# Performance work log

Measured on AMD Instinct MI355X. Metric: run time of the kernel, lower is better.

Reference implementation:

```python
import jax, jax.numpy as jnp
import numpy as np

V0, V1, V2 = 2000, 1500, 500   # diag / proc / med vocab sizes
D = 256                        # emb_dim
T = 16                         # visits per patient (query and memory)
P = 512                        # memory-bank patients
LD, LP, LM = 24, 16, 24        # codes per visit per type
PAD = V0 + V1 + V2             # padding row index (zeroed)
THRESH = 0.8
EPS = 1e-6


def setup_inputs() -> dict:
    key = jax.random.key(0)
    ks = jax.random.split(key, 16)
    inp = {
        "q_diag": jax.random.randint(ks[0], (T, LD), 0, V0),
        "q_proc": jax.random.randint(ks[1], (T, LP), 0, V1),
        "q_med": jax.random.randint(ks[2], (T, LM), 0, V2),
        "mem_diag": jax.random.randint(ks[3], (P, T, LD), 0, V0),
        "mem_proc": jax.random.randint(ks[4], (P, T, LP), 0, V1),
        "mem_med": jax.random.randint(ks[5], (P, T, LM), 0, V2),
        "emb": (jax.random.normal(ks[6], (PAD + 1, D)) * 0.05).at[PAD].set(0.0),
        "Wih": jax.random.normal(ks[7], (3 * D, D)) * 0.05,
        "Whh": jax.random.normal(ks[8], (3 * D, D)) * 0.05,
        "bih": jax.random.normal(ks[9], (3 * D,)) * 0.05,
        "bhh": jax.random.normal(ks[10], (3 * D,)) * 0.05,
        "W2": jax.random.normal(ks[11], (D, D)) * 0.05,
        "b2": jax.random.normal(ks[12], (D,)) * 0.05,
        "Wo": jax.random.normal(ks[13], (V2, D)) * 0.05,
        "bo": jax.random.normal(ks[14], (V2,)) * 0.05,
        "k": 16,
    }
    return inp


def _run_gru(x, Wih, Whh, bih, bhh):
    # x: [B, T, D]; torch nn.GRU gate order: r, z, n
    xT = jnp.swapaxes(x, 0, 1)                      # [T, B, D]
    gx = xT @ Wih.T + bih                           # [T, B, 3D]
    h0 = jnp.zeros(x.shape[:1] + x.shape[2:], x.dtype)  # [B, D]

    def step(h, gx_t):
        gh = h @ Whh.T + bhh
        xr, xz, xn = jnp.split(gx_t, 3, axis=-1)
        hr, hz, hn = jnp.split(gh, 3, axis=-1)
        r = jax.nn.sigmoid(xr + hr)
        z = jax.nn.sigmoid(xz + hz)
        n = jnp.tanh(xn + r * hn)
        h_new = (1.0 - z) * n + z * h
        return h_new, h_new

    _, hs = jax.lax.scan(step, h0, gx)
    return jnp.swapaxes(hs, 0, 1)                   # [B, T, D]


def _encode_visits(diag, proc, med, emb, Wih, Whh, bih, bhh, W2, b2):
    # diag/proc/med: [B, T, L*] int. Returns encoders for visits 1..T-1: [B, T-1, D].
    e_d = emb[diag].sum(axis=2)                     # [B, T, D]
    e_p = emb[proc + V0].sum(axis=2)
    e_m = emb[med + V0 + V1].sum(axis=2)
    e_nomed = e_d + e_p                             # current visit excludes meds
    e_full = e_nomed + e_m                          # history visits include meds
    h = _run_gru(e_full, Wih, Whh, bih, bhh)        # [B, T, D]
    # attn_g = softmax over size-1 axis == 1 exactly, so encoder_1 drops out.
    terms = jnp.tanh(h @ W2.T + b2) * e_full        # [B, T, D]
    c = jnp.cumsum(terms, axis=1)                   # prefix context sums
    return c[:, :-1] + e_nomed[:, 1:]               # enc_i = c_{i-1..} + current_i


def reference(q_diag, q_proc, q_med, mem_diag, mem_proc, mem_med,
              emb, Wih, Whh, bih, bhh, W2, b2, Wo, bo, k):
    gru = (Wih, Whh, bih, bhh)
    # Memory bank: every prefix encoder of every memory patient -> [P*(T-1), D]
    M = _encode_visits(mem_diag, mem_proc, mem_med, emb, *gru, W2, b2)
    M = M.reshape(-1, D)
    # Query patient prefix encoders -> [T-1, D]
    Q = _encode_visits(q_diag[None], q_proc[None], q_med[None], emb, *gru, W2, b2)[0]
    # Cosine similarity (torch CosineSimilarity, eps=1e-6)
    qn = jnp.maximum(jnp.linalg.norm(Q, axis=-1, keepdims=True), EPS)
    mn = jnp.maximum(jnp.linalg.norm(M, axis=-1, keepdims=True), EPS)
    sims = (Q / qn) @ (M / mn).T                    # [T-1, Nmem]
    vals, idx = jax.lax.top_k(sims, k)              # [T-1, k]
    w = jnp.where(vals > THRESH, vals, 0.0)         # threshold mask
    gathered = M[idx]                               # [T-1, k, D]
    out = Q + jnp.einsum("qk,qkd->qd", w, gathered) # weighted gather-sum
    return jax.nn.sigmoid(out @ Wo.T + bo)          # [T-1, V2]
```

## Files before the change

### kernel.cpp

```cpp
#include <hip/hip_runtime.h>
#include <math.h>

constexpr int V0_ = 2000, V1_ = 1500, V2_ = 500;
constexpr int D_ = 256, T_ = 16, P_ = 512;
constexpr int LD_ = 24, LP_ = 16, LM_ = 24;
constexpr int NPAT = P_ + 1;
constexpr int NV   = NPAT * T_;
constexpr int NM   = P_ * (T_ - 1);
constexpr int NQ   = T_ - 1;
constexpr int NROWS = NPAT * NQ;
constexpr float THRESH_ = 0.8f;
constexpr float EPS_ = 1e-6f;

__device__ __forceinline__ float sigmoidf_(float x) { return 1.0f / (1.0f + expf(-x)); }

__global__ void embed_kernel(const int* __restrict__ qd, const int* __restrict__ qp,
                             const int* __restrict__ qm, const int* __restrict__ md,
                             const int* __restrict__ mp, const int* __restrict__ mm,
                             const float* __restrict__ emb,
                             float* __restrict__ e_nomed, float* __restrict__ e_full) {
  int b = blockIdx.x;
  int p = b / T_, t = b % T_;
  int tid = threadIdx.x;
  __shared__ int codes[64];
  if (tid < 64) {
    int c;
    if (tid < LD_) {
      c = (p < P_) ? md[(p * T_ + t) * LD_ + tid] : qd[t * LD_ + tid];
    } else if (tid < LD_ + LP_) {
      int i = tid - LD_;
      c = ((p < P_) ? mp[(p * T_ + t) * LP_ + i] : qp[t * LP_ + i]) + V0_;
    } else {
      int i = tid - LD_ - LP_;
      c = ((p < P_) ? mm[(p * T_ + t) * LM_ + i] : qm[t * LM_ + i]) + V0_ + V1_;
    }
    codes[tid] = c;
  }
  __syncthreads();
  float s0 = 0.f, s1 = 0.f;
  #pragma unroll 8
  for (int i = 0; i < LD_ + LP_; ++i) s0 += emb[codes[i] * D_ + tid];
  #pragma unroll 8
  for (int i = LD_ + LP_; i < 64; ++i) s1 += emb[codes[i] * D_ + tid];
  e_nomed[(size_t)b * D_ + tid] = s0;
  e_full[(size_t)b * D_ + tid]  = s0 + s1;
}

#define BM 128
#define BN 64
#define BK 32
__global__ void gemm_nt_bias(const float* __restrict__ A, const float* __restrict__ B,
                             const float* __restrict__ bias, float* __restrict__ C,
                             int M, int N, int nct) {
  const int K = 256;
  __shared__ float As[BK][BM + 5];
  __shared__ float Bs[BK][BN + 5];
  int nb = gridDim.x;
  int b = blockIdx.x;
  int q = nb >> 3, r = nb & 7;
  int xcd = b & 7, i0 = b >> 3;
  int nbb = (xcd < r) ? (xcd * (q + 1) + i0) : (r * (q + 1) + (xcd - r) * q + i0);
  int rt = nbb / nct, ct = nbb - rt * nct;
  int r0 = rt * BM;
  int c0 = ct * BN;
  int tid = threadIdx.x;
  int tx = tid & 15, ty = tid >> 4;
  float acc[8][4];
  #pragma unroll
  for (int i = 0; i < 8; ++i)
    #pragma unroll
    for (int j = 0; j < 4; ++j) acc[i][j] = 0.f;

  for (int k0 = 0; k0 < K; k0 += BK) {
    #pragma unroll
    for (int i = 0; i < 4; ++i) {
      int flat = i * 256 + tid;
      int rr = flat >> 3;
      int kq = flat & 7;
      float4 v = make_float4(0.f, 0.f, 0.f, 0.f);
      if (r0 + rr < M) v = *(const float4*)(A + (size_t)(r0 + rr) * K + k0 + kq * 4);
      As[kq * 4 + 0][rr] = v.x; As[kq * 4 + 1][rr] = v.y;
      As[kq * 4 + 2][rr] = v.z; As[kq * 4 + 3][rr] = v.w;
    }
    #pragma unroll
    for (int i = 0; i < 2; ++i) {
      int flat = i * 256 + tid;
      int rr = flat >> 3;
      int kq = flat & 7;
      float4 v = *(const float4*)(B + (size_t)(c0 + rr) * K + k0 + kq * 4);
      Bs[kq * 4 + 0][rr] = v.x; Bs[kq * 4 + 1][rr] = v.y;
      Bs[kq * 4 + 2][rr] = v.z; Bs[kq * 4 + 3][rr] = v.w;
    }
    __syncthreads();
    #pragma unroll
    for (int kk = 0; kk < BK; ++kk) {
      float4 a0 = *(const float4*)&As[kk][ty * 8];
      float4 a1 = *(const float4*)&As[kk][ty * 8 + 4];
      float4 bv = *(const float4*)&Bs[kk][tx * 4];
      float av[8] = {a0.x, a0.y, a0.z, a0.w, a1.x, a1.y, a1.z, a1.w};
      float bw[4] = {bv.x, bv.y, bv.z, bv.w};
      #pragma unroll
      for (int i = 0; i < 8; ++i)
        #pragma unroll
        for (int j = 0; j < 4; ++j) acc[i][j] = fmaf(av[i], bw[j], acc[i][j]);
    }
    __syncthreads();
  }
  float bv0 = bias[c0 + tx * 4 + 0], bv1 = bias[c0 + tx * 4 + 1];
  float bv2 = bias[c0 + tx * 4 + 2], bv3 = bias[c0 + tx * 4 + 3];
  #pragma unroll
  for (int i = 0; i < 8; ++i) {
    int rr = r0 + ty * 8 + i;
    if (rr < M) {
      float4 o = make_float4(acc[i][0] + bv0, acc[i][1] + bv1,
                             acc[i][2] + bv2, acc[i][3] + bv3);
      *(float4*)(C + (size_t)rr * N + c0 + tx * 4) = o;
    }
  }
}

__global__ void transpose_whh(const float* __restrict__ Whh, float* __restrict__ WT) {
  int idx = blockIdx.x * 256 + threadIdx.x;
  int row = idx >> 8;
  int e = idx & 255;
  WT[e * 768 + row] = Whh[idx];
}

__global__ __launch_bounds__(512) void gru_all(const float* __restrict__ gx,
                                               const float* __restrict__ WT,
                                               const float* __restrict__ bhh,
                                               float* __restrict__ hs_all) {
  int tid = threadIdx.x;
  int d = tid & 255;
  int hf = tid >> 8;
  int p0 = blockIdx.x * 3;
  __shared__ float hL[3][D_];
  __shared__ float part[9][D_];
  if (hf == 0) { hL[0][d] = 0.f; hL[1][d] = 0.f; hL[2][d] = 0.f; }
  float brd = bhh[d], bzd = bhh[D_ + d], bnd = bhh[2 * D_ + d];
  __syncthreads();

  for (int t = 0; t < T_; ++t) {
    float ar[3] = {0.f, 0.f, 0.f}, az[3] = {0.f, 0.f, 0.f}, an[3] = {0.f, 0.f, 0.f};
    const float* wt = WT + d;
    int e0 = hf << 7;
    #pragma unroll 4
    for (int e = e0; e < e0 + 128; ++e) {
      const float* we = wt + (size_t)e * 768;
      float w0 = we[0];
      float w1 = we[256];
      float w2 = we[512];
      float h0 = hL[0][e], h1 = hL[1][e], h2 = hL[2][e];
      ar[0] = fmaf(h0, w0, ar[0]); az[0] = fmaf(h0, w1, az[0]); an[0] = fmaf(h0, w2, an[0]);
      ar[1] = fmaf(h1, w0, ar[1]); az[1] = fmaf(h1, w1, az[1]); an[1] = fmaf(h1, w2, an[1]);
      ar[2] = fmaf(h2, w0, ar[2]); az[2] = fmaf(h2, w1, az[2]); an[2] = fmaf(h2, w2, an[2]);
    }
    if (hf == 1) {
      #pragma unroll
      for (int i = 0; i < 3; ++i) {
        part[i][d] = ar[i]; part[3 + i][d] = az[i]; part[6 + i][d] = an[i];
      }
    }
    __syncthreads();
    if (hf == 0) {
      #pragma unroll
      for (int i = 0; i < 3; ++i) {
        int p = p0 + i;
        const float* gxp = gx + (size_t)(p * T_ + t) * 768;
        float r = sigmoidf_(gxp[d] + brd + ar[i] + part[i][d]);
        float z = sigmoidf_(gxp[D_ + d] + bzd + az[i] + part[3 + i][d]);
        float n = tanhf(gxp[2 * D_ + d] + r * (an[i] + part[6 + i][d] + bnd));
        float hn = (1.f - z) * n + z * hL[i][d];
        hL[i][d] = hn;
        hs_all[(size_t)(p * T_ + t) * D_ + d] = hn;
      }
    }
    __syncthreads();
  }
}

__global__ void enc_kernel(const float* __restrict__ tmp, const float* __restrict__ e_full,
                           const float* __restrict__ e_nomed, float* __restrict__ enc) {
  int p = blockIdx.x, d = threadIdx.x;
  float acc = 0.f;
  for (int t = 0; t < NQ; ++t) {
    size_t vi = (size_t)(p * T_ + t) * D_ + d;
    acc += tanhf(tmp[vi]) * e_full[vi];
    enc[(size_t)(p * NQ + t) * D_ + d] = acc + e_nomed[(size_t)(p * T_ + t + 1) * D_ + d];
  }
}

__global__ void norm_kernel(const float* __restrict__ enc, float* __restrict__ norms) {
  int row = blockIdx.x * 4 + (threadIdx.x >> 6);
  int lane = threadIdx.x & 63;
  if (row >= NROWS) return;
  const float* rp = enc + (size_t)row * D_;
  float s = 0.f;
  #pragma unroll
  for (int i = 0; i < 4; ++i) { float v = rp[lane + i * 64]; s += v * v; }
  #pragma unroll
  for (int off = 32; off > 0; off >>= 1) s += __shfl_down(s, off, 64);
  if (lane == 0) norms[row] = fmaxf(sqrtf(s), EPS_);
}

__global__ void sims_kernel(const float* __restrict__ enc, const float* __restrict__ norms,
                            float* __restrict__ sims) {
  int q = blockIdx.y;
  int m = blockIdx.x * 256 + threadIdx.x;
  __shared__ float qs[D_];
  qs[threadIdx.x] = enc[(size_t)(NM + q) * D_ + threadIdx.x];
  __syncthreads();
  const float* mrow = enc + (size_t)m * D_;
  float dot = 0.f;
  #pragma unroll 8
  for (int e = 0; e < D_; e += 4) {
    float4 a = *(const float4*)(qs + e);
    float4 b = *(const float4*)(mrow + e);
    dot += a.x * b.x + a.y * b.y + a.z * b.z + a.w * b.w;
  }
  sims[(size_t)q * NM + m] = dot / (norms[NM + q] * norms[m]);
}

#define CAP 4096
__global__ void topk_gather(const float* __restrict__ sims, const float* __restrict__ enc,
                            const int* __restrict__ kptr, float* __restrict__ outq) {
  int q = blockIdx.x, tid = threadIdx.x;
  __shared__ int cnt;
  __shared__ float cv[CAP];
  __shared__ int ci[CAP];
  __shared__ float selv[64];
  __shared__ int seli[64];
  __shared__ float rv[256];
  __shared__ int ri[256];
  if (tid == 0) cnt = 0;
  __syncthreads();
  const float* sq = sims + (size_t)q * NM;
  for (int j = tid; j < NM; j += 256) {
    float v = sq[j];
    if (v > THRESH_) {
      int slot = atomicAdd(&cnt, 1);
      if (slot < CAP) { cv[slot] = v; ci[slot] = j; }
    }
  }
  __syncthreads();
  int k = kptr[0];
  if (k > 64) k = 64;
  if (k < 0) k = 0;
  int n = cnt; if (n > CAP) n = CAP;
  int nsel;
  if (n <= k) {
    nsel = n;
    if (tid < n) { selv[tid] = cv[tid]; seli[tid] = ci[tid]; }
  } else {
    nsel = k;
    for (int it = 0; it < k; ++it) {
      float best = -3e38f; int bslot = -1;
      for (int j = tid; j < n; j += 256) {
        float v = cv[j];
        if (v > best) { best = v; bslot = j; }
        else if (v == best && bslot >= 0 && ci[j] < ci[bslot]) { bslot = j; }
      }
      rv[tid] = best; ri[tid] = bslot;
      __syncthreads();
      for (int off = 128; off > 0; off >>= 1) {
        if (tid < off) {
          float v2 = rv[tid + off]; int s2 = ri[tid + off];
          if (s2 >= 0 && (ri[tid] < 0 || v2 > rv[tid] ||
                          (v2 == rv[tid] && ci[s2] < ci[ri[tid]]))) {
            rv[tid] = v2; ri[tid] = s2;
          }
        }
        __syncthreads();
      }
      if (tid == 0) {
        int s = ri[0];
        selv[it] = rv[0]; seli[it] = ci[s];
        cv[s] = -3e38f;
      }
      __syncthreads();
    }
  }
  __syncthreads();
  float o = enc[(size_t)(NM + q) * D_ + tid];
  for (int j = 0; j < nsel; ++j)
    o += selv[j] * enc[(size_t)seli[j] * D_ + tid];
  outq[(size_t)q * D_ + tid] = o;
}

__global__ void out_kernel(const float* __restrict__ outq, const float* __restrict__ Wo,
                           const float* __restrict__ bo, float* __restrict__ out) {
  int q = blockIdx.y;
  int v = blockIdx.x * 256 + threadIdx.x;
  __shared__ float qs[D_];
  qs[threadIdx.x] = outq[(size_t)q * D_ + threadIdx.x];
  __syncthreads();
  if (v >= V2_) return;
  const float* wr = Wo + (size_t)v * D_;
  float dot = bo[v];
  #pragma unroll 8
  for (int e = 0; e < D_; e += 4) {
    float4 a = *(const float4*)(qs + e);
    float4 b = *(const float4*)(wr + e);
    dot += a.x * b.x + a.y * b.y + a.z * b.z + a.w * b.w;
  }
  out[(size_t)q * V2_ + v] = 1.f / (1.f + expf(-dot));
}

extern "C" void kernel_launch(void* const* d_in, const int* in_sizes, int n_in,
                              void* d_out, int out_size, void* d_ws, size_t ws_size,
                              hipStream_t stream) {
  const int* qd = (const int*)d_in[0];
  const int* qp = (const int*)d_in[1];
  const int* qm = (const int*)d_in[2];
  const int* md = (const int*)d_in[3];
  const int* mp = (const int*)d_in[4];
  const int* mm = (const int*)d_in[5];
  const float* emb = (const float*)d_in[6];
  const float* Wih = (const float*)d_in[7];
  const float* Whh = (const float*)d_in[8];
  const float* bih = (const float*)d_in[9];
  const float* bhh = (const float*)d_in[10];
  const float* W2  = (const float*)d_in[11];
  const float* b2  = (const float*)d_in[12];
  const float* Wo  = (const float*)d_in[13];
  const float* bo  = (const float*)d_in[14];
  const int* kptr  = (const int*)d_in[15];
  float* out = (float*)d_out;
  (void)in_sizes; (void)n_in; (void)out_size; (void)ws_size;

  char* ws = (char*)d_ws;
  size_t off = 0;
  auto alloc = [&](size_t nfloats) {
    float* pp = (float*)(ws + off);
    off += ((nfloats * sizeof(float) + 255) & ~(size_t)255);
    return pp;
  };
  float* e_full  = alloc((size_t)NV * D_);
  float* e_nomed = alloc((size_t)NV * D_);
  float* gx      = alloc((size_t)NV * 768);
  float* hs_all  = alloc((size_t)NV * D_);
  float* tmp     = alloc((size_t)NV * D_);
  float* enc     = alloc((size_t)NROWS * D_);
  float* norms   = alloc(NROWS);
  float* sims    = alloc((size_t)NQ * NM);
  float* outq    = alloc((size_t)NQ * D_);
  float* WT      = alloc((size_t)256 * 768);

  embed_kernel<<<NV, 256, 0, stream>>>(qd, qp, qm, md, mp, mm, emb, e_nomed, e_full);

  transpose_whh<<<768, 256, 0, stream>>>(Whh, WT);

  {
    int nrt = (NV + BM - 1) / BM, nct = 768 / BN;
    gemm_nt_bias<<<nrt * nct, 256, 0, stream>>>(e_full, Wih, bih, gx, NV, 768, nct);
  }

  gru_all<<<NPAT / 3, 512, 0, stream>>>(gx, WT, bhh, hs_all);

  {
    int nrt = (NV + BM - 1) / BM, nct = 256 / BN;
    gemm_nt_bias<<<nrt * nct, 256, 0, stream>>>(hs_all, W2, b2, tmp, NV, 256, nct);
  }

  enc_kernel<<<NPAT, 256, 0, stream>>>(tmp, e_full, e_nomed, enc);
  norm_kernel<<<(NROWS + 3) / 4, 256, 0, stream>>>(enc, norms);
  sims_kernel<<<dim3(NM / 256, NQ), 256, 0, stream>>>(enc, norms, sims);
  topk_gather<<<NQ, 256, 0, stream>>>(sims, enc, kptr, outq);
  out_kernel<<<dim3((V2_ + 255) / 256, NQ), 256, 0, stream>>>(outq, Wo, bo, out);
}
```

Before: 408.5 us.

## Vectorize GRU recurrent weights as float4, split K four ways, fuse norm into encoder

The transposed recurrent weight matrix is re-laid out into float4 groups so each GRU thread loads four k-values per gate at once, and the hidden-state reads from shared memory become float4. The recurrent matvec now splits K across four 256-thread quarters in 1024-thread blocks instead of two, with three partial-sum slabs reduced in shared memory. The row-norm computation moves into the encoder kernel through a wave shuffle plus block reduction, which removes one launch and a re-read of the encodings. In exchange the GRU uses more shared memory and larger blocks, and the encoder loop adds two barriers per step.

New measurement: 387.9 us. 5.0% less time.

```diff
diff --git a/kernel.cpp b/kernel.cpp
--- a/kernel.cpp
+++ b/kernel.cpp
@@ -119,57 +119,68 @@
   }
 }
 
-__global__ void transpose_whh(const float* __restrict__ Whh, float* __restrict__ WT) {
-  int idx = blockIdx.x * 256 + threadIdx.x;
-  int row = idx >> 8;
-  int e = idx & 255;
-  WT[e * 768 + row] = Whh[idx];
-}
-
-__global__ __launch_bounds__(512) void gru_all(const float* __restrict__ gx,
-                                               const float* __restrict__ WT,
-                                               const float* __restrict__ bhh,
-                                               float* __restrict__ hs_all) {
+__global__ void transpose_whh(const float* __restrict__ Whh, float* __restrict__ WT4) {
+  int b = blockIdx.x;
+  int e4 = b / 3, g = b - e4 * 3;
+  int d = threadIdx.x;
+  float4 v = *(const float4*)(Whh + ((size_t)(g * 256 + d)) * 256 + e4 * 4);
+  *((float4*)WT4 + (size_t)b * 256 + d) = v;
+}
+
+__global__ __launch_bounds__(1024) void gru_all(const float* __restrict__ gx,
+                                                const float* __restrict__ WT4,
+                                                const float* __restrict__ bhh,
+                                                float* __restrict__ hs_all) {
   int tid = threadIdx.x;
   int d = tid & 255;
-  int hf = tid >> 8;
+  int qt = tid >> 8;
   int p0 = blockIdx.x * 3;
   __shared__ float hL[3][D_];
-  __shared__ float part[9][D_];
-  if (hf == 0) { hL[0][d] = 0.f; hL[1][d] = 0.f; hL[2][d] = 0.f; }
+  __shared__ float part[3][9][D_];
+  if (qt == 0) { hL[0][d] = 0.f; hL[1][d] = 0.f; hL[2][d] = 0.f; }
   float brd = bhh[d], bzd = bhh[D_ + d], bnd = bhh[2 * D_ + d];
   __syncthreads();
 
+  const float4* wt = (const float4*)WT4 + d;
   for (int t = 0; t < T_; ++t) {
     float ar[3] = {0.f, 0.f, 0.f}, az[3] = {0.f, 0.f, 0.f}, an[3] = {0.f, 0.f, 0.f};
-    const float* wt = WT + d;
-    int e0 = hf << 7;
+    int e40 = qt << 4;
     #pragma unroll 4
-    for (int e = e0; e < e0 + 128; ++e) {
-      const float* we = wt + (size_t)e * 768;
-      float w0 = we[0];
-      float w1 = we[256];
-      float w2 = we[512];
-      float h0 = hL[0][e], h1 = hL[1][e], h2 = hL[2][e];
-      ar[0] = fmaf(h0, w0, ar[0]); az[0] = fmaf(h0, w1, az[0]); an[0] = fmaf(h0, w2, an[0]);
-      ar[1] = fmaf(h1, w0, ar[1]); az[1] = fmaf(h1, w1, az[1]); an[1] = fmaf(h1, w2, an[1]);
-      ar[2] = fmaf(h2, w0, ar[2]); az[2] = fmaf(h2, w1, az[2]); an[2] = fmaf(h2, w2, an[2]);
-    }
-    if (hf == 1) {
+    for (int e4 = e40; e4 < e40 + 16; ++e4) {
+      const float4* wb = wt + (size_t)(e4 * 3) * 256;
+      float4 w0 = wb[0];
+      float4 w1 = wb[256];
+      float4 w2 = wb[512];
       #pragma unroll
       for (int i = 0; i < 3; ++i) {
-        part[i][d] = ar[i]; part[3 + i][d] = az[i]; part[6 + i][d] = an[i];
-      }
-    }
-    __syncthreads();
-    if (hf == 0) {
+        float4 h4 = *(const float4*)&hL[i][e4 << 2];
+        ar[i] = fmaf(h4.x, w0.x, ar[i]); ar[i] = fmaf(h4.y, w0.y, ar[i]);
+        ar[i] = fmaf(h4.z, w0.z, ar[i]); ar[i] = fmaf(h4.w, w0.w, ar[i]);
+        az[i] = fmaf(h4.x, w1.x, az[i]); az[i] = fmaf(h4.y, w1.y, az[i]);
+        az[i] = fmaf(h4.z, w1.z, az[i]); az[i] = fmaf(h4.w, w1.w, az[i]);
+        an[i] = fmaf(h4.x, w2.x, an[i]); an[i] = fmaf(h4.y, w2.y, an[i]);
+        an[i] = fmaf(h4.z, w2.z, an[i]); an[i] = fmaf(h4.w, w2.w, an[i]);
+      }
+    }
+    if (qt) {
+      int s = qt - 1;
+      #pragma unroll
+      for (int i = 0; i < 3; ++i) {
+        part[s][i][d] = ar[i]; part[s][3 + i][d] = az[i]; part[s][6 + i][d] = an[i];
+      }
+    }
+    __syncthreads();
+    if (qt == 0) {
       #pragma unroll
       for (int i = 0; i < 3; ++i) {
         int p = p0 + i;
         const float* gxp = gx + (size_t)(p * T_ + t) * 768;
-        float r = sigmoidf_(gxp[d] + brd + ar[i] + part[i][d]);
-        float z = sigmoidf_(gxp[D_ + d] + bzd + az[i] + part[3 + i][d]);
-        float n = tanhf(gxp[2 * D_ + d] + r * (an[i] + part[6 + i][d] + bnd));
+        float arf = ar[i] + part[0][i][d] + part[1][i][d] + part[2][i][d];
+        float azf = az[i] + part[0][3 + i][d] + part[1][3 + i][d] + part[2][3 + i][d];
+        float anf = an[i] + part[0][6 + i][d] + part[1][6 + i][d] + part[2][6 + i][d];
+        float r = sigmoidf_(gxp[d] + brd + arf);
+        float z = sigmoidf_(gxp[D_ + d] + bzd + azf);
+        float n = tanhf(gxp[2 * D_ + d] + r * (anf + bnd));
         float hn = (1.f - z) * n + z * hL[i][d];
         hL[i][d] = hn;
         hs_all[(size_t)(p * T_ + t) * D_ + d] = hn;
@@ -180,27 +191,25 @@
 }
 
 __global__ void enc_kernel(const float* __restrict__ tmp, const float* __restrict__ e_full,
-                           const float* __restrict__ e_nomed, float* __restrict__ enc) {
+                           const float* __restrict__ e_nomed, float* __restrict__ enc,
+                           float* __restrict__ norms) {
   int p = blockIdx.x, d = threadIdx.x;
+  __shared__ float red[4];
   float acc = 0.f;
   for (int t = 0; t < NQ; ++t) {
     size_t vi = (size_t)(p * T_ + t) * D_ + d;
     acc += tanhf(tmp[vi]) * e_full[vi];
-    enc[(size_t)(p * NQ + t) * D_ + d] = acc + e_nomed[(size_t)(p * T_ + t + 1) * D_ + d];
-  }
-}
-
-__global__ void norm_kernel(const float* __restrict__ enc, float* __restrict__ norms) {
-  int row = blockIdx.x * 4 + (threadIdx.x >> 6);
-  int lane = threadIdx.x & 63;
-  if (row >= NROWS) return;
-  const float* rp = enc + (size_t)row * D_;
-  float s = 0.f;
-  #pragma unroll
-  for (int i = 0; i < 4; ++i) { float v = rp[lane + i * 64]; s += v * v; }
-  #pragma unroll
-  for (int off = 32; off > 0; off >>= 1) s += __shfl_down(s, off, 64);
-  if (lane == 0) norms[row] = fmaxf(sqrtf(s), EPS_);
+    float ev = acc + e_nomed[(size_t)(p * T_ + t + 1) * D_ + d];
+    int row = p * NQ + t;
+    enc[(size_t)row * D_ + d] = ev;
+    float s = ev * ev;
+    #pragma unroll
+    for (int off = 32; off > 0; off >>= 1) s += __shfl_down(s, off, 64);
+    if ((d & 63) == 0) red[d >> 6] = s;
+    __syncthreads();
+    if (d == 0) norms[row] = fmaxf(sqrtf(red[0] + red[1] + red[2] + red[3]), EPS_);
+    __syncthreads();
+  }
 }
 
 __global__ void sims_kernel(const float* __restrict__ enc, const float* __restrict__ norms,
@@ -344,26 +353,25 @@
   float* norms   = alloc(NROWS);
   float* sims    = alloc((size_t)NQ * NM);
   float* outq    = alloc((size_t)NQ * D_);
-  float* WT      = alloc((size_t)256 * 768);
+  float* WT4     = alloc((size_t)256 * 768);
 
   embed_kernel<<<NV, 256, 0, stream>>>(qd, qp, qm, md, mp, mm, emb, e_nomed, e_full);
 
-  transpose_whh<<<768, 256, 0, stream>>>(Whh, WT);
+  transpose_whh<<<192, 256, 0, stream>>>(Whh, WT4);
 
   {
     int nrt = (NV + BM - 1) / BM, nct = 768 / BN;
     gemm_nt_bias<<<nrt * nct, 256, 0, stream>>>(e_full, Wih, bih, gx, NV, 768, nct);
   }
 
-  gru_all<<<NPAT / 3, 512, 0, stream>>>(gx, WT, bhh, hs_all);
+  gru_all<<<NPAT / 3, 1024, 0, stream>>>(gx, WT4, bhh, hs_all);
 
   {
     int nrt = (NV + BM - 1) / BM, nct = 256 / BN;
     gemm_nt_bias<<<nrt * nct, 256, 0, stream>>>(hs_all, W2, b2, tmp, NV, 256, nct);
   }
 
-  enc_kernel<<<NPAT, 256, 0, stream>>>(tmp, e_full, e_nomed, enc);
-  norm_kernel<<<(NROWS + 3) / 4, 256, 0, stream>>>(enc, norms);
+  enc_kernel<<<NPAT, 256, 0, stream>>>(tmp, e_full, e_nomed, enc, norms);
   sims_kernel<<<dim3(NM / 256, NQ), 256, 0, stream>>>(enc, norms, sims);
   topk_gather<<<NQ, 256, 0, stream>>>(sims, enc, kptr, outq);
   out_kernel<<<dim3((V2_ + 255) / 256, NQ), 256, 0, stream>>>(outq, Wo, bo, out);
```
